# Optimization experiments

Measured on AMD Instinct MI355X. Metric: run time of the kernel, lower is better.

## Reference

```python
import jax, jax.numpy as jnp
import numpy as np

LN_EPS = 1e-6          # flax nn.LayerNorm default
ATTN_EPS = 1e-9        # numerical_stabilizer default


def ln_points(x, scale, bias):
    """flax LayerNorm(reduction_axes=-2): stats over points axis, affine over feature axis."""
    mu = jnp.mean(x, axis=-2, keepdims=True)
    var = jnp.mean(jnp.square(x), axis=-2, keepdims=True) - jnp.square(mu)
    return (x - mu) * jax.lax.rsqrt(var + LN_EPS) * scale + bias


def self_attention_layer(x, wq_i, bq_i, wk_i, bk_i, wv_i, bv_i, wo_i, bo_i, ls_i, lb_i):
    # 1x1 convs == pointwise linears
    q = x @ wq_i + bq_i                                  # [B,N,C]
    k = x @ wk_i + bk_i
    v = x @ wv_i + bv_i
    attn = jnp.einsum('bmc,bnc->bmn', q, k)              # [B,M,N]
    attn = jax.nn.softmax(attn, axis=-1)
    # extra offset-attention renorm: divide by column sums (axis=1)
    attn = attn / (ATTN_EPS + jnp.sum(attn, axis=1, keepdims=True))
    # einsum '...MN,...NC->...NC' reduces M: scales v by column sums
    col = jnp.sum(attn, axis=1)                          # [B,N]
    out = col[..., None] * v                             # [B,N,C]
    out = out @ wo_i + bo_i
    out = jax.nn.relu(ln_points(out, ls_i, lb_i))
    return out + x


def setup_inputs() -> dict:
    key = jax.random.key(0)
    ks = jax.random.split(key, 16)
    B, N, IN, C, F, L = 2, 4096, 3, 256, 1024, 4
    s_in = 1.0 / np.sqrt(IN)
    s_c = 1.0 / np.sqrt(C)
    s_f = 1.0 / np.sqrt(L * C)
    return {
        'inputs': jax.random.normal(ks[0], (B, N, IN), jnp.float32),
        'w0': jax.random.normal(ks[1], (IN, C), jnp.float32) * s_in,
        'b0': jnp.zeros((C,), jnp.float32),
        'ln0_s': jnp.ones((C,), jnp.float32),
        'ln0_b': jnp.zeros((C,), jnp.float32),
        'w1': jax.random.normal(ks[2], (C, C), jnp.float32) * s_c,
        'b1': jnp.zeros((C,), jnp.float32),
        'ln1_s': jnp.ones((C,), jnp.float32),
        'ln1_b': jnp.zeros((C,), jnp.float32),
        'wq': jax.random.normal(ks[3], (L, C, C), jnp.float32) * s_c,
        'bq': jnp.zeros((L, C), jnp.float32),
        'wk': jax.random.normal(ks[4], (L, C, C), jnp.float32) * s_c,
        'bk': jnp.zeros((L, C), jnp.float32),
        'wv': jax.random.normal(ks[5], (L, C, C), jnp.float32) * s_c,
        'bv': jnp.zeros((L, C), jnp.float32),
        'wo': jax.random.normal(ks[6], (L, C, C), jnp.float32) * s_c,
        'bo': jnp.zeros((L, C), jnp.float32),
        'attn_ln_s': jnp.ones((L, C), jnp.float32),
        'attn_ln_b': jnp.zeros((L, C), jnp.float32),
        'wf': jax.random.normal(ks[7], (L * C, F), jnp.float32) * s_f,
        'bf': jnp.zeros((F,), jnp.float32),
    }


def reference(inputs, w0, b0, ln0_s, ln0_b, w1, b1, ln1_s, ln1_b,
              wq, bq, wk, bk, wv, bv, wo, bo, attn_ln_s, attn_ln_b, wf, bf):
    # pre-conv stack
    out = ln_points(inputs @ w0 + b0, ln0_s, ln0_b)
    out = ln_points(out @ w1 + b1, ln1_s, ln1_b)
    # attention stack (4 structurally identical layers, concatenated)
    attn_outs = []
    for i in range(wq.shape[0]):
        out = self_attention_layer(out, wq[i], bq[i], wk[i], bk[i],
                                   wv[i], bv[i], wo[i], bo[i],
                                   attn_ln_s[i], attn_ln_b[i])
        attn_outs.append(out)
    out = jnp.concatenate(attn_outs, axis=-1)            # [B,N,4C]
    out = out @ wf + bf                                  # [B,N,F]
    return out
```

## Files before the change

### kernel.cpp

```cpp
#include <hip/hip_runtime.h>

#define BB 2
#define NN 4096
#define CC 256
#define FF 1024
#define NLAYER 4
#define RR (BB*NN)
#define SPL 16
#define QKLD (3*CC)
#define NEG_BIG (-1e30f)
#define LOG2E 1.44269504f

typedef _Float16 h16;
typedef __attribute__((ext_vector_type(8))) _Float16 half8;
typedef __attribute__((ext_vector_type(4))) float f32x4;
typedef __attribute__((ext_vector_type(16))) float f32x16;

#define WAITVM(n) asm volatile("s_waitcnt vmcnt(" #n ")" ::: "memory")

__device__ __forceinline__ void gload16(const h16* g, h16* l) {
    __builtin_amdgcn_global_load_lds((const __attribute__((address_space(1))) void*)g,
                                     (__attribute__((address_space(3))) void*)l, 16, 0, 0);
}

template<int ROWS>
__device__ __forceinline__ void stage_rows(const h16* __restrict__ src, int ld,
    int row0, int c0, h16* lds, int tid)
{
    int w = tid >> 6;
    #pragma unroll
    for (int t = 0; t < ROWS/32; ++t) {
        int slot = t*256 + tid;
        int row = slot >> 3;
        int pp  = slot & 7;
        int piece = pp ^ (row & 7);
        gload16(src + (size_t)(row0 + row)*ld + c0 + piece*8,
                lds + (t*256 + w*64)*8);
    }
}

__device__ __forceinline__ half8 frag_ld(const h16* lds, int row, int pl) {
    return *(const half8*)(lds + row*64 + ((pl ^ (row & 7))*8));
}

__global__ __launch_bounds__(256) void pct_wtrans(const float* __restrict__ W,
    h16* __restrict__ WT, int K, int N, int dstride, float scale)
{
    __shared__ h16 t[32][33];
    const float* Wl = W + (size_t)blockIdx.z*K*N;
    h16* WTl = WT + (size_t)blockIdx.z*dstride;
    int k0 = blockIdx.x*32, n0 = blockIdx.y*32;
    int tx = threadIdx.x & 31, ty = threadIdx.x >> 5;
    #pragma unroll
    for (int i = ty; i < 32; i += 8)
        t[i][tx] = (h16)(Wl[(size_t)(k0+i)*N + n0 + tx] * scale);
    __syncthreads();
    #pragma unroll
    for (int i = ty; i < 32; i += 8)
        WTl[(size_t)(n0+i)*K + k0 + tx] = t[tx][i];
}

__global__ __launch_bounds__(256) void pct_wtrans_qkv(const float* __restrict__ wq,
    const float* __restrict__ wk, const float* __restrict__ wv,
    const float* __restrict__ bq, const float* __restrict__ bk, const float* __restrict__ bv,
    h16* __restrict__ WT, float* __restrict__ bqkv)
{
    __shared__ h16 t[32][33];
    int z = blockIdx.z;
    int which = z >> 2, layer = z & 3;
    const float* Wl = (which == 0 ? wq : which == 1 ? wk : wv) + (size_t)layer*CC*CC;
    h16* WTl = WT + (size_t)layer*QKLD*CC + (size_t)which*CC*CC;
    float scale = (which == 0) ? LOG2E : 1.0f;
    int k0 = blockIdx.x*32, n0 = blockIdx.y*32;
    int tx = threadIdx.x & 31, ty = threadIdx.x >> 5;
    #pragma unroll
    for (int i = ty; i < 32; i += 8)
        t[i][tx] = (h16)(Wl[(size_t)(k0+i)*CC + n0 + tx] * scale);
    if (blockIdx.x == 0 && blockIdx.y == 0) {
        const float* bsrc = (which == 0 ? bq : which == 1 ? bk : bv);
        bqkv[layer*QKLD + which*CC + threadIdx.x] = bsrc[layer*CC + threadIdx.x] * scale;
    }
    __syncthreads();
    #pragma unroll
    for (int i = ty; i < 32; i += 8)
        WTl[(size_t)(n0+i)*CC + k0 + tx] = t[tx][i];
}

__global__ __launch_bounds__(256) void pct_wfold(const float* __restrict__ w1,
    const float* __restrict__ sums, const float* __restrict__ ls, const float* __restrict__ lb,
    const float* __restrict__ b1, h16* __restrict__ w1Tb, float* __restrict__ biasb)
{
    __shared__ h16 t[32][33];
    __shared__ float bb[8][32];
    int b = blockIdx.z;
    int k0 = blockIdx.x*32, n0 = blockIdx.y*32;
    int tx = threadIdx.x & 31, ty = threadIdx.x >> 5;
    float psum = 0.f;
    #pragma unroll
    for (int i = ty; i < 32; i += 8) {
        int k = k0 + i;
        float s1 = sums[(b*CC + k)*2], s2 = sums[(b*CC + k)*2 + 1];
        float mu  = s1 * (1.f/NN);
        float var = s2 * (1.f/NN) - mu*mu;
        float rstd = rsqrtf(var + 1e-6f);
        float A = rstd * ls[k];
        float Bv = lb[k] - mu * rstd * ls[k];
        float wv = w1[(size_t)k*CC + n0 + tx];
        t[i][tx] = (h16)(wv * A);
        psum += Bv * wv;
    }
    bb[ty][tx] = psum;
    __syncthreads();
    if (ty == 0) {
        float s = 0.f;
        #pragma unroll
        for (int r = 0; r < 8; ++r) s += bb[r][tx];
        if (k0 == 0) s += b1[n0 + tx];
        atomicAdd(&biasb[b*CC + n0 + tx], s);
    }
    #pragma unroll
    for (int i = ty; i < 32; i += 8)
        w1Tb[(size_t)b*CC*CC + (size_t)(n0+i)*CC + k0 + tx] = t[tx][i];
}

__global__ __launch_bounds__(256) void pct_embed(const float* __restrict__ inp,
    const float* __restrict__ w0, const float* __restrict__ b0,
    h16* __restrict__ out, float* __restrict__ sums)
{
    int c = threadIdx.x;
    int r0 = blockIdx.x * 64;
    float wa = w0[c], wb = w0[CC+c], wcv = w0[2*CC+c], bb = b0[c];
    float s1 = 0.f, s2 = 0.f;
    #pragma unroll 4
    for (int i = 0; i < 64; ++i) {
        int r = r0 + i;
        float y = bb + inp[r*3+0]*wa + inp[r*3+1]*wb + inp[r*3+2]*wcv;
        h16 hy = (h16)y;
        out[(size_t)r*CC + c] = hy;
        float yf = (float)hy;
        s1 += yf; s2 += yf*yf;
    }
    int b = r0 >> 12;
    atomicAdd(&sums[((size_t)b*CC + c)*2 + 0], s1);
    atomicAdd(&sums[((size_t)b*CC + c)*2 + 1], s2);
}

__global__ __launch_bounds__(256) void pct_lnapply(const h16* __restrict__ x, int ldx,
    const float* __restrict__ sums, const float* __restrict__ scale, const float* __restrict__ bias,
    const h16* __restrict__ res, int ldr, h16* __restrict__ out, int ldo,
    int do_relu)
{
    int r = blockIdx.x*8 + (threadIdx.x >> 5);
    int cg = (threadIdx.x & 31) * 8;
    int b = r / NN;
    half8 xv = *(const half8*)(x + (size_t)r*ldx + cg);
    half8 rv;
    if (res) rv = *(const half8*)(res + (size_t)r*ldr + cg);
    half8 ov;
    #pragma unroll
    for (int j = 0; j < 8; ++j) {
        int c = cg + j;
        float s1 = sums[(b*CC + c)*2], s2 = sums[(b*CC + c)*2 + 1];
        float mu  = s1 * (1.f/NN);
        float var = s2 * (1.f/NN) - mu*mu;
        float rstd = rsqrtf(var + 1e-6f);
        float y = ((float)xv[j] - mu) * rstd * scale[c] + bias[c];
        if (do_relu) y = fmaxf(y, 0.f);
        if (res) y += (float)rv[j];
        ov[j] = (h16)y;
    }
    *(half8*)(out + (size_t)r*ldo + cg) = ov;
}

template<int BN, bool OUT_F32, bool CSTAT>
__global__ __launch_bounds__(256) void pct_gemm_f16(
    const h16* __restrict__ A, int lda,
    const h16* __restrict__ WT, const float* __restrict__ bias,
    void* __restrict__ outp, int ldo, int K, const float* __restrict__ rowS,
    float* __restrict__ csums, int wbs, int bbs)
{
    constexpr int BJ = BN/2;
    constexpr int NF = BJ/16;
    __shared__ __align__(16) h16 Asm[128*64];
    __shared__ __align__(16) h16 Bsm[BN*64];
    const int tid = threadIdx.x;
    const int lane = tid & 63, w = tid >> 6;
    const int ln = lane & 15, lq = lane >> 4;
    const int wr = w >> 1, wc = w & 1;
    const int m0 = blockIdx.x*128, n0 = blockIdx.y*BN;
    WT   += (size_t)(m0 >> 12) * wbs;
    bias += (size_t)(m0 >> 12) * bbs;
    f32x4 acc[4][NF];
    #pragma unroll
    for (int i = 0; i < 4; ++i)
        #pragma unroll
        for (int j = 0; j < NF; ++j) acc[i][j] = (f32x4){0.f,0.f,0.f,0.f};
    for (int k0 = 0; k0 < K; k0 += 64) {
        stage_rows<128>(A, lda, m0, k0, Asm, tid);
        stage_rows<BN>(WT, K, n0, k0, Bsm, tid);
        __syncthreads();
        #pragma unroll
        for (int kk = 0; kk < 2; ++kk) {
            half8 af[4], bfr[NF];
            #pragma unroll
            for (int i = 0; i < 4; ++i) af[i] = frag_ld(Asm, wr*64 + i*16 + ln, kk*4 + lq);
            #pragma unroll
            for (int j = 0; j < NF; ++j) bfr[j] = frag_ld(Bsm, wc*BJ + j*16 + ln, kk*4 + lq);
            #pragma unroll
            for (int i = 0; i < 4; ++i)
                #pragma unroll
                for (int j = 0; j < NF; ++j)
                    acc[i][j] = __builtin_amdgcn_mfma_f32_16x16x32_f16(af[i], bfr[j], acc[i][j], 0, 0, 0);
        }
        __syncthreads();
    }
    float cs1[NF], cs2[NF];
    #pragma unroll
    for (int j = 0; j < NF; ++j) {
        int col = n0 + wc*BJ + j*16 + ln;
        float bv = bias[col];
        float s1 = 0.f, s2 = 0.f;
        #pragma unroll
        for (int i = 0; i < 4; ++i) {
            #pragma unroll
            for (int r = 0; r < 4; ++r) {
                int row = m0 + wr*64 + i*16 + lq*4 + r;
                float sc = 1.f;
                if (rowS) { float s = rowS[row]; sc = s / (1e-9f + s); }
                float v = acc[i][j][r] * sc + bv;
                if (OUT_F32) ((float*)outp)[(size_t)row*ldo + col] = v;
                else ((h16*)outp)[(size_t)row*ldo + col] = (h16)v;
                if (CSTAT) { s1 += v; s2 += v*v; }
            }
        }
        cs1[j] = s1; cs2[j] = s2;
    }
    if constexpr (CSTAT) {
        __shared__ float cred[2][2][BJ][2];
        #pragma unroll
        for (int j = 0; j < NF; ++j) {
            float s1 = cs1[j], s2 = cs2[j];
            s1 += __shfl_down(s1, 16); s1 += __shfl_down(s1, 32);
            s2 += __shfl_down(s2, 16); s2 += __shfl_down(s2, 32);
            if (lane < 16) {
                cred[wr][wc][j*16 + lane][0] = s1;
                cred[wr][wc][j*16 + lane][1] = s2;
            }
        }
        __syncthreads();
        if (tid < 2*BN) {
            int c = tid >> 1, st = tid & 1;
            int wcc = c >> 5, ci = c & 31;
            float v = cred[0][wcc][ci][st] + cred[1][wcc][ci][st];
            int b = m0 >> 12;
            atomicAdd(&csums[((size_t)b*CC + n0 + c)*2 + st], v);
        }
    }
}

__global__ __launch_bounds__(256) void attn_rowstats(const h16* __restrict__ QKV,
    float2* __restrict__ part)
{
    __shared__ __align__(16) h16 Ks[2][128*64];
    const int b = blockIdx.x, mt = blockIdx.y, sp = blockIdx.z;
    const int tid = threadIdx.x;
    const int lane = tid & 63, w = tid >> 6;
    const int ln2 = lane & 31, h = lane >> 5;
    const h16* qb = QKV + (size_t)b*NN*QKLD;
    const h16* kb = qb + CC;
    const int m0 = mt*128;
    const h16* qrow = qb + (size_t)(m0 + w*32 + ln2)*QKLD + h*8;
    half8 qreg[16];
    #pragma unroll
    for (int i = 0; i < 16; ++i) qreg[i] = *(const half8*)(qrow + i*16);

    const int nbeg = sp*(NN/SPL);
    constexpr int NT = (NN/SPL)/128;
    constexpr int NCH = NT*4;
    float rm = NEG_BIG, rs = 0.f;

    stage_rows<128>(kb, QKLD, nbeg, 0, Ks[0], tid);
    int id = 0;
    #pragma unroll
    for (int t = 0; t < NT; ++t) {
        f32x16 acc[4];
        #pragma unroll
        for (int j = 0; j < 4; ++j) acc[j] = (f32x16)(0.f);
        #pragma unroll
        for (int c = 0; c < 4; ++c, ++id) {
            if (id + 1 < NCH) {
                stage_rows<128>(kb, QKLD, nbeg + ((id+1) >> 2)*128, ((id+1) & 3)*64,
                                Ks[(id+1) & 1], tid);
                WAITVM(4);
            } else {
                WAITVM(0);
            }
            __builtin_amdgcn_s_barrier();
            const h16* buf = Ks[id & 1];
            __builtin_amdgcn_s_setprio(1);
            #pragma unroll
            for (int kk = 0; kk < 4; ++kk) {
                half8 bq = qreg[c*4 + kk];
                #pragma unroll
                for (int j = 0; j < 4; ++j) {
                    half8 af = frag_ld(buf, j*32 + ln2, kk*2 + h);
                    acc[j] = __builtin_amdgcn_mfma_f32_32x32x16_f16(af, bq, acc[j], 0, 0, 0);
                }
            }
            __builtin_amdgcn_s_setprio(0);
            __builtin_amdgcn_s_barrier();
        }
        float tm = NEG_BIG;
        #pragma unroll
        for (int j = 0; j < 4; ++j)
            #pragma unroll
            for (int g = 0; g < 16; g += 2)
                tm = fmaxf(tm, fmaxf(acc[j][g], acc[j][g+1]));
        if (tm > rm) { rs *= exp2f(rm - tm); rm = tm; }
        float s = 0.f;
        #pragma unroll
        for (int j = 0; j < 4; ++j)
            #pragma unroll
            for (int g = 0; g < 16; ++g)
                s += exp2f(acc[j][g] - rm);
        rs += s;
    }
    float mo = __shfl_xor(rm, 32, 64);
    float so = __shfl_xor(rs, 32, 64);
    float mn = fmaxf(rm, mo);
    float sm = rs*exp2f(rm - mn) + so*exp2f(mo - mn);
    if (lane < 32) {
        int m = m0 + w*32 + ln2;
        part[((size_t)b*NN + m)*SPL + sp] = make_float2(mn, sm);
    }
}

__global__ __launch_bounds__(256) void attn_colsums(const h16* __restrict__ QKV,
    const float2* __restrict__ part, float* __restrict__ S)
{
    __shared__ __align__(16) h16 Qs[2][128*64];
    __shared__ float rst_d[256];
    const int b = blockIdx.x, nt = blockIdx.y, sp = blockIdx.z;
    const int tid = threadIdx.x;
    const int lane = tid & 63, w = tid >> 6;
    const int ln2 = lane & 31, h = lane >> 5;
    const h16* qb = QKV + (size_t)b*NN*QKLD;
    const h16* kb = qb + CC;
    const int n0 = nt*128;
    const int mbeg = sp*(NN/SPL);

    {
        const float4* pp4 = (const float4*)(part + ((size_t)b*NN + mbeg + tid)*SPL);
        float4 v[SPL/2];
        #pragma unroll
        for (int i = 0; i < SPL/2; ++i) v[i] = pp4[i];
        float m = NEG_BIG;
        #pragma unroll
        for (int i = 0; i < SPL/2; ++i) m = fmaxf(m, fmaxf(v[i].x, v[i].z));
        float sum = 0.f;
        #pragma unroll
        for (int i = 0; i < SPL/2; ++i) {
            sum += v[i].y * exp2f(v[i].x - m);
            sum += v[i].w * exp2f(v[i].z - m);
        }
        rst_d[tid] = -m - __log2f(sum);
    }
    __syncthreads();

    const h16* krow = kb + (size_t)(n0 + w*32 + ln2)*QKLD + h*8;
    half8 kreg[16];
    #pragma unroll
    for (int i = 0; i < 16; ++i) kreg[i] = *(const half8*)(krow + i*16);

    constexpr int NT = (NN/SPL)/128;
    constexpr int NCH = NT*4;
    float cs = 0.f;

    stage_rows<128>(qb, QKLD, mbeg, 0, Qs[0], tid);
    int id = 0;
    #pragma unroll
    for (int t = 0; t < NT; ++t) {
        f32x16 acc[4];
        #pragma unroll
        for (int j = 0; j < 4; ++j) acc[j] = (f32x16)(0.f);
        #pragma unroll
        for (int c = 0; c < 4; ++c, ++id) {
            if (id + 1 < NCH) {
                stage_rows<128>(qb, QKLD, mbeg + ((id+1) >> 2)*128, ((id+1) & 3)*64,
                                Qs[(id+1) & 1], tid);
                WAITVM(4);
            } else {
                WAITVM(0);
            }
            __builtin_amdgcn_s_barrier();
            const h16* buf = Qs[id & 1];
            __builtin_amdgcn_s_setprio(1);
            #pragma unroll
            for (int kk = 0; kk < 4; ++kk) {
                half8 bk = kreg[c*4 + kk];
                #pragma unroll
                for (int j = 0; j < 4; ++j) {
                    half8 af = frag_ld(buf, j*32 + ln2, kk*2 + h);
                    acc[j] = __builtin_amdgcn_mfma_f32_32x32x16_f16(af, bk, acc[j], 0, 0, 0);
                }
            }
            __builtin_amdgcn_s_setprio(0);
            __builtin_amdgcn_s_barrier();
        }
        int mt0 = t*128;
        #pragma unroll
        for (int j = 0; j < 4; ++j) {
            #pragma unroll
            for (int g = 0; g < 16; ++g) {
                int mloc = mt0 + j*32 + (g & 3) + 8*(g >> 2) + 4*h;
                cs += exp2f(acc[j][g] + rst_d[mloc]);
            }
        }
    }
    cs += __shfl_xor(cs, 32, 64);
    if (lane < 32) {
        int n = n0 + w*32 + ln2;
        atomicAdd(&S[(size_t)b*NN + n], cs);
    }
}

extern "C" void kernel_launch(void* const* d_in, const int* in_sizes, int n_in,
                              void* d_out, int out_size, void* d_ws, size_t ws_size,
                              hipStream_t stream)
{
    const float* inp  = (const float*)d_in[0];
    const float* w0   = (const float*)d_in[1];
    const float* b0   = (const float*)d_in[2];
    const float* ln0s = (const float*)d_in[3];
    const float* ln0b = (const float*)d_in[4];
    const float* w1   = (const float*)d_in[5];
    const float* b1   = (const float*)d_in[6];
    const float* ln1s = (const float*)d_in[7];
    const float* ln1b = (const float*)d_in[8];
    const float* wq   = (const float*)d_in[9];
    const float* bq   = (const float*)d_in[10];
    const float* wk   = (const float*)d_in[11];
    const float* bk   = (const float*)d_in[12];
    const float* wv   = (const float*)d_in[13];
    const float* bv   = (const float*)d_in[14];
    const float* wo   = (const float*)d_in[15];
    const float* bo   = (const float*)d_in[16];
    const float* alns = (const float*)d_in[17];
    const float* alnb = (const float*)d_in[18];
    const float* wf   = (const float*)d_in[19];
    const float* bfb  = (const float*)d_in[20];
    float* out = (float*)d_out;

    char* p = (char*)d_ws;
    auto alloc = [&](size_t bytes) { char* r = p; p += (bytes + 255) & ~255ULL; return r; };
    h16* t0    = (h16*)alloc((size_t)RR*CC*2);
    h16* t2    = (h16*)alloc((size_t)RR*CC*2);
    h16* x1    = (h16*)alloc((size_t)RR*CC*2);
    h16* qkv   = (h16*)alloc((size_t)RR*QKLD*2);
    h16* oh    = (h16*)alloc((size_t)RR*CC*2);
    h16* xcat  = (h16*)alloc((size_t)RR*FF*2);
    h16* w1Tb  = (h16*)alloc((size_t)BB*CC*CC*2);
    h16* wqkvT = (h16*)alloc((size_t)NLAYER*QKLD*CC*2);
    h16* woT   = (h16*)alloc((size_t)NLAYER*CC*CC*2);
    h16* wfT   = (h16*)alloc((size_t)FF*FF*2);
    float* bqkv  = (float*)alloc((size_t)NLAYER*QKLD*4);
    float2* part  = (float2*)alloc((size_t)RR*SPL*8);
    float* Ssum  = (float*)alloc((size_t)NLAYER*RR*4);
    float* lns   = (float*)alloc((size_t)6*BB*CC*2*4);
    float* biasb = (float*)alloc((size_t)BB*CC*4);

    dim3 blk(256);

    hipMemsetAsync(Ssum, 0, (size_t)((char*)(biasb + BB*CC) - (char*)Ssum), stream);

    pct_wtrans_qkv<<<dim3(CC/32, CC/32, 3*NLAYER), blk, 0, stream>>>(
        wq, wk, wv, bq, bk, bv, wqkvT, bqkv);
    pct_wtrans<<<dim3(CC/32, CC/32, NLAYER), blk, 0, stream>>>(wo, woT, CC, CC, CC*CC, 1.f);
    pct_wtrans<<<dim3(FF/32, FF/32, 1), blk, 0, stream>>>(wf, wfT, FF, FF, FF*FF, 1.f);

    pct_embed<<<RR/64, blk, 0, stream>>>(inp, w0, b0, t0, lns + 0*BB*CC*2);
    pct_wfold<<<dim3(CC/32, CC/32, BB), blk, 0, stream>>>(
        w1, lns + 0*BB*CC*2, ln0s, ln0b, b1, w1Tb, biasb);
    pct_gemm_f16<64,false,true><<<dim3(RR/128, CC/64), blk, 0, stream>>>(
        t0, CC, w1Tb, biasb, t2, CC, CC, nullptr, lns + 1*BB*CC*2, CC*CC, CC);
    pct_lnapply<<<RR/8, blk, 0, stream>>>(t2, CC, lns + 1*BB*CC*2, ln1s, ln1b, nullptr, 0, x1, CC, 0);

    const h16* xin = x1; int ldx = CC;
    for (int i = 0; i < NLAYER; ++i) {
        pct_gemm_f16<64,false,false><<<dim3(RR/128, QKLD/64), blk, 0, stream>>>(
            xin, ldx, wqkvT + (size_t)i*QKLD*CC, bqkv + i*QKLD, qkv, QKLD, CC, nullptr, nullptr, 0, 0);

        attn_rowstats<<<dim3(BB, NN/128, SPL), blk, 0, stream>>>(qkv, part);
        attn_colsums<<<dim3(BB, NN/128, SPL), blk, 0, stream>>>(qkv, part, Ssum + (size_t)i*RR);

        pct_gemm_f16<64,false,true><<<dim3(RR/128, CC/64), blk, 0, stream>>>(
            qkv + 2*CC, QKLD, woT + (size_t)i*CC*CC, bo + i*CC, oh, CC, CC,
            Ssum + (size_t)i*RR, lns + (2+i)*BB*CC*2, 0, 0);

        pct_lnapply<<<RR/8, blk, 0, stream>>>(oh, CC, lns + (2+i)*BB*CC*2, alns + i*CC, alnb + i*CC,
                                              xin, ldx, xcat + i*CC, FF, 1);
        xin = xcat + i*CC; ldx = FF;
    }

    pct_gemm_f16<128,true,false><<<dim3(RR/128, FF/128), blk, 0, stream>>>(
        xcat, FF, wfT, bfb, out, FF, FF, nullptr, nullptr, 0, 0);
}
```

Before: 501.8 us.

## Retile attention row/column-stat kernels to 256x256 blocks with 512 threads

Result: slower. 609.7 us (+21.5%).

```diff
diff --git a/kernel.cpp b/kernel.cpp
--- a/kernel.cpp
+++ b/kernel.cpp
@@ -6,7 +6,6 @@
 #define FF 1024
 #define NLAYER 4
 #define RR (BB*NN)
-#define SPL 16
 #define QKLD (3*CC)
 #define NEG_BIG (-1e30f)
 #define LOG2E 1.44269504f
@@ -14,7 +13,6 @@
 typedef _Float16 h16;
 typedef __attribute__((ext_vector_type(8))) _Float16 half8;
 typedef __attribute__((ext_vector_type(4))) float f32x4;
-typedef __attribute__((ext_vector_type(16))) float f32x16;
 
 #define WAITVM(n) asm volatile("s_waitcnt vmcnt(" #n ")" ::: "memory")
 
@@ -23,19 +21,19 @@
                                      (__attribute__((address_space(3))) void*)l, 16, 0, 0);
 }
 
-template<int ROWS>
+template<int ROWS, int THREADS>
 __device__ __forceinline__ void stage_rows(const h16* __restrict__ src, int ld,
     int row0, int c0, h16* lds, int tid)
 {
     int w = tid >> 6;
     #pragma unroll
-    for (int t = 0; t < ROWS/32; ++t) {
-        int slot = t*256 + tid;
+    for (int t = 0; t < (ROWS*8)/THREADS; ++t) {
+        int slot = t*THREADS + tid;
         int row = slot >> 3;
         int pp  = slot & 7;
         int piece = pp ^ (row & 7);
         gload16(src + (size_t)(row0 + row)*ld + c0 + piece*8,
-                lds + (t*256 + w*64)*8);
+                lds + (t*THREADS + w*64)*8);
     }
 }
 
@@ -196,8 +194,8 @@
         #pragma unroll
         for (int j = 0; j < NF; ++j) acc[i][j] = (f32x4){0.f,0.f,0.f,0.f};
     for (int k0 = 0; k0 < K; k0 += 64) {
-        stage_rows<128>(A, lda, m0, k0, Asm, tid);
-        stage_rows<BN>(WT, K, n0, k0, Bsm, tid);
+        stage_rows<128,256>(A, lda, m0, k0, Asm, tid);
+        stage_rows<BN,256>(WT, K, n0, k0, Bsm, tid);
         __syncthreads();
         #pragma unroll
         for (int kk = 0; kk < 2; ++kk) {
@@ -258,169 +256,176 @@
     }
 }
 
-__global__ __launch_bounds__(256) void attn_rowstats(const h16* __restrict__ QKV,
+__global__ __launch_bounds__(512, 2) void attn_rowstats(const h16* __restrict__ QKV,
     float2* __restrict__ part)
 {
-    __shared__ __align__(16) h16 Ks[2][128*64];
-    const int b = blockIdx.x, mt = blockIdx.y, sp = blockIdx.z;
+    __shared__ __align__(16) h16 SM[2][2][256*64];
+    const int b = blockIdx.x, mt = blockIdx.y, nt = blockIdx.z;
     const int tid = threadIdx.x;
     const int lane = tid & 63, w = tid >> 6;
-    const int ln2 = lane & 31, h = lane >> 5;
+    const int ln = lane & 15, lq = lane >> 4;
+    const int wm = w >> 2, wn = w & 3;
     const h16* qb = QKV + (size_t)b*NN*QKLD;
     const h16* kb = qb + CC;
-    const int m0 = mt*128;
-    const h16* qrow = qb + (size_t)(m0 + w*32 + ln2)*QKLD + h*8;
-    half8 qreg[16];
-    #pragma unroll
-    for (int i = 0; i < 16; ++i) qreg[i] = *(const half8*)(qrow + i*16);
-
-    const int nbeg = sp*(NN/SPL);
-    constexpr int NT = (NN/SPL)/128;
-    constexpr int NCH = NT*4;
-    float rm = NEG_BIG, rs = 0.f;
-
-    stage_rows<128>(kb, QKLD, nbeg, 0, Ks[0], tid);
-    int id = 0;
-    #pragma unroll
-    for (int t = 0; t < NT; ++t) {
-        f32x16 acc[4];
-        #pragma unroll
-        for (int j = 0; j < 4; ++j) acc[j] = (f32x16)(0.f);
-        #pragma unroll
-        for (int c = 0; c < 4; ++c, ++id) {
-            if (id + 1 < NCH) {
-                stage_rows<128>(kb, QKLD, nbeg + ((id+1) >> 2)*128, ((id+1) & 3)*64,
-                                Ks[(id+1) & 1], tid);
-                WAITVM(4);
-            } else {
-                WAITVM(0);
+    const int m0 = mt*256, n0 = nt*256;
+
+    f32x4 acc[8][4];
+    #pragma unroll
+    for (int mi = 0; mi < 8; ++mi)
+        #pragma unroll
+        for (int ni = 0; ni < 4; ++ni) acc[mi][ni] = (f32x4){0.f,0.f,0.f,0.f};
+
+    stage_rows<256,512>(qb, QKLD, m0, 0, SM[0][0], tid);
+    stage_rows<256,512>(kb, QKLD, n0, 0, SM[0][1], tid);
+    for (int s = 0; s < 4; ++s) {
+        if (s + 1 < 4) {
+            stage_rows<256,512>(qb, QKLD, m0, (s+1)*64, SM[(s+1)&1][0], tid);
+            stage_rows<256,512>(kb, QKLD, n0, (s+1)*64, SM[(s+1)&1][1], tid);
+            WAITVM(8);
+        } else {
+            WAITVM(0);
+        }
+        __builtin_amdgcn_s_barrier();
+        const h16* bufA = SM[s&1][0];
+        const h16* bufB = SM[s&1][1];
+        __builtin_amdgcn_s_setprio(1);
+        #pragma unroll
+        for (int kk = 0; kk < 2; ++kk) {
+            half8 af[8], bf[4];
+            #pragma unroll
+            for (int mi = 0; mi < 8; ++mi)
+                af[mi] = frag_ld(bufA, wm*128 + mi*16 + ln, kk*4 + lq);
+            #pragma unroll
+            for (int ni = 0; ni < 4; ++ni)
+                bf[ni] = frag_ld(bufB, wn*64 + ni*16 + ln, kk*4 + lq);
+            #pragma unroll
+            for (int mi = 0; mi < 8; ++mi)
+                #pragma unroll
+                for (int ni = 0; ni < 4; ++ni)
+                    acc[mi][ni] = __builtin_amdgcn_mfma_f32_16x16x32_f16(
+                        af[mi], bf[ni], acc[mi][ni], 0, 0, 0);
+        }
+        __builtin_amdgcn_s_setprio(0);
+        __builtin_amdgcn_s_barrier();
+    }
+    #pragma unroll
+    for (int mi = 0; mi < 8; ++mi) {
+        #pragma unroll
+        for (int r = 0; r < 4; ++r) {
+            float lm = fmaxf(fmaxf(acc[mi][0][r], acc[mi][1][r]),
+                             fmaxf(acc[mi][2][r], acc[mi][3][r]));
+            lm = fmaxf(lm, __shfl_xor(lm, 1, 64));
+            lm = fmaxf(lm, __shfl_xor(lm, 2, 64));
+            lm = fmaxf(lm, __shfl_xor(lm, 4, 64));
+            lm = fmaxf(lm, __shfl_xor(lm, 8, 64));
+            float lsv = exp2f(acc[mi][0][r] - lm) + exp2f(acc[mi][1][r] - lm)
+                      + exp2f(acc[mi][2][r] - lm) + exp2f(acc[mi][3][r] - lm);
+            lsv += __shfl_xor(lsv, 1, 64);
+            lsv += __shfl_xor(lsv, 2, 64);
+            lsv += __shfl_xor(lsv, 4, 64);
+            lsv += __shfl_xor(lsv, 8, 64);
+            if (ln == mi) {
+                int m = m0 + wm*128 + mi*16 + lq*4 + r;
+                part[((size_t)b*NN + m)*64 + nt*4 + wn] = make_float2(lm, lsv);
             }
-            __builtin_amdgcn_s_barrier();
-            const h16* buf = Ks[id & 1];
-            __builtin_amdgcn_s_setprio(1);
-            #pragma unroll
-            for (int kk = 0; kk < 4; ++kk) {
-                half8 bq = qreg[c*4 + kk];
-                #pragma unroll
-                for (int j = 0; j < 4; ++j) {
-                    half8 af = frag_ld(buf, j*32 + ln2, kk*2 + h);
-                    acc[j] = __builtin_amdgcn_mfma_f32_32x32x16_f16(af, bq, acc[j], 0, 0, 0);
-                }
-            }
-            __builtin_amdgcn_s_setprio(0);
-            __builtin_amdgcn_s_barrier();
-        }
-        float tm = NEG_BIG;
-        #pragma unroll
-        for (int j = 0; j < 4; ++j)
-            #pragma unroll
-            for (int g = 0; g < 16; g += 2)
-                tm = fmaxf(tm, fmaxf(acc[j][g], acc[j][g+1]));
-        if (tm > rm) { rs *= exp2f(rm - tm); rm = tm; }
-        float s = 0.f;
-        #pragma unroll
-        for (int j = 0; j < 4; ++j)
-            #pragma unroll
-            for (int g = 0; g < 16; ++g)
-                s += exp2f(acc[j][g] - rm);
-        rs += s;
-    }
-    float mo = __shfl_xor(rm, 32, 64);
-    float so = __shfl_xor(rs, 32, 64);
-    float mn = fmaxf(rm, mo);
-    float sm = rs*exp2f(rm - mn) + so*exp2f(mo - mn);
-    if (lane < 32) {
-        int m = m0 + w*32 + ln2;
-        part[((size_t)b*NN + m)*SPL + sp] = make_float2(mn, sm);
-    }
-}
-
-__global__ __launch_bounds__(256) void attn_colsums(const h16* __restrict__ QKV,
+        }
+    }
+}
+
+__global__ __launch_bounds__(512, 2) void attn_colsums(const h16* __restrict__ QKV,
     const float2* __restrict__ part, float* __restrict__ S)
 {
-    __shared__ __align__(16) h16 Qs[2][128*64];
+    __shared__ __align__(16) h16 SM[2][2][256*64];
     __shared__ float rst_d[256];
-    const int b = blockIdx.x, nt = blockIdx.y, sp = blockIdx.z;
+    const int b = blockIdx.x, mt = blockIdx.y, nt = blockIdx.z;
     const int tid = threadIdx.x;
     const int lane = tid & 63, w = tid >> 6;
-    const int ln2 = lane & 31, h = lane >> 5;
+    const int ln = lane & 15, lq = lane >> 4;
+    const int wm = w >> 2, wn = w & 3;
     const h16* qb = QKV + (size_t)b*NN*QKLD;
     const h16* kb = qb + CC;
-    const int n0 = nt*128;
-    const int mbeg = sp*(NN/SPL);
-
-    {
-        const float4* pp4 = (const float4*)(part + ((size_t)b*NN + mbeg + tid)*SPL);
-        float4 v[SPL/2];
-        #pragma unroll
-        for (int i = 0; i < SPL/2; ++i) v[i] = pp4[i];
+    const int m0 = mt*256, n0 = nt*256;
+
+    stage_rows<256,512>(qb, QKLD, m0, 0, SM[0][0], tid);
+    stage_rows<256,512>(kb, QKLD, n0, 0, SM[0][1], tid);
+
+    if (tid < 256) {
+        const float4* pp4 = (const float4*)(part + ((size_t)b*NN + m0 + tid)*64);
         float m = NEG_BIG;
-        #pragma unroll
-        for (int i = 0; i < SPL/2; ++i) m = fmaxf(m, fmaxf(v[i].x, v[i].z));
+        #pragma unroll 8
+        for (int i = 0; i < 32; ++i) {
+            float4 v = pp4[i];
+            m = fmaxf(m, fmaxf(v.x, v.z));
+        }
         float sum = 0.f;
-        #pragma unroll
-        for (int i = 0; i < SPL/2; ++i) {
-            sum += v[i].y * exp2f(v[i].x - m);
-            sum += v[i].w * exp2f(v[i].z - m);
+        #pragma unroll 8
+        for (int i = 0; i < 32; ++i) {
+            float4 v = pp4[i];
+            sum += v.y * exp2f(v.x - m) + v.w * exp2f(v.z - m);
         }
         rst_d[tid] = -m - __log2f(sum);
     }
     __syncthreads();
 
-    const h16* krow = kb + (size_t)(n0 + w*32 + ln2)*QKLD + h*8;
-    half8 kreg[16];
-    #pragma unroll
-    for (int i = 0; i < 16; ++i) kreg[i] = *(const half8*)(krow + i*16);
-
-    constexpr int NT = (NN/SPL)/128;
-    constexpr int NCH = NT*4;
-    float cs = 0.f;
-
-    stage_rows<128>(qb, QKLD, mbeg, 0, Qs[0], tid);
-    int id = 0;
-    #pragma unroll
-    for (int t = 0; t < NT; ++t) {
-        f32x16 acc[4];
-        #pragma unroll
-        for (int j = 0; j < 4; ++j) acc[j] = (f32x16)(0.f);
-        #pragma unroll
-        for (int c = 0; c < 4; ++c, ++id) {
-            if (id + 1 < NCH) {
-                stage_rows<128>(qb, QKLD, mbeg + ((id+1) >> 2)*128, ((id+1) & 3)*64,
-                                Qs[(id+1) & 1], tid);
-                WAITVM(4);
-            } else {
-                WAITVM(0);
-            }
-            __builtin_amdgcn_s_barrier();
-            const h16* buf = Qs[id & 1];
-            __builtin_amdgcn_s_setprio(1);
-            #pragma unroll
-            for (int kk = 0; kk < 4; ++kk) {
-                half8 bk = kreg[c*4 + kk];
+    f32x4 acc[8][4];
+    #pragma unroll
+    for (int mi = 0; mi < 8; ++mi)
+        #pragma unroll
+        for (int ni = 0; ni < 4; ++ni) acc[mi][ni] = (f32x4){0.f,0.f,0.f,0.f};
+
+    for (int s = 0; s < 4; ++s) {
+        if (s + 1 < 4) {
+            stage_rows<256,512>(qb, QKLD, m0, (s+1)*64, SM[(s+1)&1][0], tid);
+            stage_rows<256,512>(kb, QKLD, n0, (s+1)*64, SM[(s+1)&1][1], tid);
+            WAITVM(8);
+        } else {
+            WAITVM(0);
+        }
+        __builtin_amdgcn_s_barrier();
+        const h16* bufA = SM[s&1][0];
+        const h16* bufB = SM[s&1][1];
+        __builtin_amdgcn_s_setprio(1);
+        #pragma unroll
+        for (int kk = 0; kk < 2; ++kk) {
+            half8 af[8], bf[4];
+            #pragma unroll
+            for (int mi = 0; mi < 8; ++mi)
+                af[mi] = frag_ld(bufA, wm*128 + mi*16 + ln, kk*4 + lq);
+            #pragma unroll
+            for (int ni = 0; ni < 4; ++ni)
+                bf[ni] = frag_ld(bufB, wn*64 + ni*16 + ln, kk*4 + lq);
+            #pragma unroll
+            for (int mi = 0; mi < 8; ++mi)
                 #pragma unroll
-                for (int j = 0; j < 4; ++j) {
-                    half8 af = frag_ld(buf, j*32 + ln2, kk*2 + h);
-                    acc[j] = __builtin_amdgcn_mfma_f32_32x32x16_f16(af, bk, acc[j], 0, 0, 0);
-                }
-            }
-            __builtin_amdgcn_s_setprio(0);
-            __builtin_amdgcn_s_barrier();
-        }
-        int mt0 = t*128;
-        #pragma unroll
-        for (int j = 0; j < 4; ++j) {
-            #pragma unroll
-            for (int g = 0; g < 16; ++g) {
-                int mloc = mt0 + j*32 + (g & 3) + 8*(g >> 2) + 4*h;
-                cs += exp2f(acc[j][g] + rst_d[mloc]);
-            }
-        }
-    }
-    cs += __shfl_xor(cs, 32, 64);
-    if (lane < 32) {
-        int n = n0 + w*32 + ln2;
-        atomicAdd(&S[(size_t)b*NN + n], cs);
+                for (int ni = 0; ni < 4; ++ni)
+                    acc[mi][ni] = __builtin_amdgcn_mfma_f32_16x16x32_f16(
+                        af[mi], bf[ni], acc[mi][ni], 0, 0, 0);
+        }
+        __builtin_amdgcn_s_setprio(0);
+        __builtin_amdgcn_s_barrier();
+    }
+    float cs[4] = {0.f, 0.f, 0.f, 0.f};
+    #pragma unroll
+    for (int mi = 0; mi < 8; ++mi) {
+        #pragma unroll
+        for (int r = 0; r < 4; ++r) {
+            float dv = rst_d[wm*128 + mi*16 + lq*4 + r];
+            #pragma unroll
+            for (int ni = 0; ni < 4; ++ni)
+                cs[ni] += exp2f(acc[mi][ni][r] + dv);
+        }
+    }
+    #pragma unroll
+    for (int ni = 0; ni < 4; ++ni) {
+        cs[ni] += __shfl_xor(cs[ni], 16, 64);
+        cs[ni] += __shfl_xor(cs[ni], 32, 64);
+    }
+    if (lq == 0) {
+        #pragma unroll
+        for (int ni = 0; ni < 4; ++ni) {
+            int n = n0 + wn*64 + ni*16 + ln;
+            atomicAdd(&S[(size_t)b*NN + n], cs[ni]);
+        }
     }
 }
 
@@ -464,7 +469,7 @@
     h16* woT   = (h16*)alloc((size_t)NLAYER*CC*CC*2);
     h16* wfT   = (h16*)alloc((size_t)FF*FF*2);
     float* bqkv  = (float*)alloc((size_t)NLAYER*QKLD*4);
-    float2* part  = (float2*)alloc((size_t)RR*SPL*8);
+    float2* part  = (float2*)alloc((size_t)RR*64*8);
     float* Ssum  = (float*)alloc((size_t)NLAYER*RR*4);
     float* lns   = (float*)alloc((size_t)6*BB*CC*2*4);
     float* biasb = (float*)alloc((size_t)BB*CC*4);
@@ -490,8 +495,8 @@
         pct_gemm_f16<64,false,false><<<dim3(RR/128, QKLD/64), blk, 0, stream>>>(
             xin, ldx, wqkvT + (size_t)i*QKLD*CC, bqkv + i*QKLD, qkv, QKLD, CC, nullptr, nullptr, 0, 0);
 
-        attn_rowstats<<<dim3(BB, NN/128, SPL), blk, 0, stream>>>(qkv, part);
-        attn_colsums<<<dim3(BB, NN/128, SPL), blk, 0, stream>>>(qkv, part, Ssum + (size_t)i*RR);
+        attn_rowstats<<<dim3(BB, NN/256, NN/256), dim3(512), 0, stream>>>(qkv, part);
+        attn_colsums<<<dim3(BB, NN/256, NN/256), dim3(512), 0, stream>>>(qkv, part, Ssum + (size_t)i*RR);
 
         pct_gemm_f16<64,false,true><<<dim3(RR/128, CC/64), blk, 0, stream>>>(
             qkv + 2*CC, QKLD, woT + (size_t)i*CC*CC, bo + i*CC, oh, CC, CC,
```
